# Optimization experiments

Measured on AMD Instinct MI355X. Metric: run time of the kernel, lower is better.

The kernel has to match this reference:

```python
import jax, jax.numpy as jnp
import numpy as np

B, S, HID = 2, 4096, 2048
H, D = 16, 128
BS = 64            # block_size
SR = 0.5           # sparsity_ratio
NB = S // BS       # number of diagonal blocks
SCALE = D ** -0.5


def setup_inputs() -> dict:
    key = jax.random.key(0)
    ks = jax.random.split(key, 7)
    s = 0.02
    return {
        "hidden_states": jax.random.normal(ks[0], (B, S, HID), jnp.float32),
        "Wq": jax.random.normal(ks[1], (HID, H * D), jnp.float32) * s,
        "Wk": jax.random.normal(ks[2], (HID, H * D), jnp.float32) * s,
        "Wv": jax.random.normal(ks[3], (HID, H * D), jnp.float32) * s,
        "Wo": jax.random.normal(ks[4], (H * D, HID), jnp.float32) * s,
        "Wr": jax.random.normal(ks[5], (HID, H), jnp.float32) * s,   # block_router weight
        "br": jax.random.normal(ks[6], (H,), jnp.float32) * s,       # block_router bias
    }


def reference(hidden_states, Wq, Wk, Wv, Wo, Wr, br):
    # projections: torch Linear(x) == x @ W^T; weights stored pre-transposed here
    q = (hidden_states @ Wq).reshape(B, S, H, D).transpose(0, 2, 1, 3)  # [B,H,S,D]
    k = (hidden_states @ Wk).reshape(B, S, H, D).transpose(0, 2, 1, 3)
    v = (hidden_states @ Wv).reshape(B, S, H, D).transpose(0, 2, 1, 3)

    # per-head routing score, mean-pooled over batch (as in torch: routing_scores[:, h].mean())
    routing = jax.nn.sigmoid(hidden_states.mean(axis=1) @ Wr + br)      # [B,H]
    head_score = routing.mean(axis=0)                                   # [H]
    eff_sparsity = SR * (1.0 - head_score * 0.5)
    # torch: max(1, int(block_size * eff)); positive -> floor == int truncation
    attend_count = jnp.maximum(1, jnp.floor(BS * eff_sparsity).astype(jnp.int32))  # [H]

    # block-diagonal attention: only within-block scores are ever finite, so we
    # never materialize the full SxS matrix (softmax over -inf elsewhere is a no-op)
    qb = q.reshape(B, H, NB, BS, D)
    kb = k.reshape(B, H, NB, BS, D)
    vb = v.reshape(B, H, NB, BS, D)
    scores = jnp.einsum("bhnqd,bhnkd->bhnqk", qb, kb) * SCALE           # [B,H,NB,BS,BS]

    # rank of each key within its row (descending); keep == variable-k top-k mask.
    order = jnp.argsort(-scores, axis=-1)
    rank = jnp.argsort(order, axis=-1)
    keep = rank < attend_count[None, :, None, None, None]
    # non-top-k in-block entries are scattered as 0.0 (not -inf) in the original
    masked = jnp.where(keep, scores, 0.0)

    probs = jax.nn.softmax(masked.astype(jnp.float32), axis=-1).astype(q.dtype)
    out_b = jnp.einsum("bhnqk,bhnkd->bhnqd", probs, vb)                 # [B,H,NB,BS,D]
    out = out_b.reshape(B, H, S, D).transpose(0, 2, 1, 3).reshape(B, S, H * D)
    return out @ Wo
```

## Files before the change

kernel.cpp:

```cpp
#include <hip/hip_runtime.h>
#include <hip/hip_bf16.h>
#include <cstdint>
#include <cstddef>

#define B_   2
#define S_   4096
#define HIDN 2048
#define H_   16
#define D_   128
#define NB_  64
#define MTOT 8192
#define QKVN 6144
#define SCALE_ 0.08838834764831845f

typedef unsigned short ushort_t;
typedef __attribute__((ext_vector_type(8))) short short8;
typedef __attribute__((ext_vector_type(8))) ushort_t ushort8;
typedef __attribute__((ext_vector_type(4))) float f32x4;

__device__ inline float b2f(ushort_t x){ union{unsigned u; float f;} v; v.u=((unsigned)x)<<16; return v.f; }
__device__ inline ushort_t f2b(float f){ union{unsigned u; float f;} v; v.f=f; unsigned r=(v.u + 0x7FFF + ((v.u>>16)&1))>>16; return (ushort_t)r; }

#define MFMA_BF16(a,b,c) __builtin_amdgcn_mfma_f32_16x16x32_bf16((a),(b),(c),0,0,0)

__device__ inline void async16(const ushort_t* g, ushort_t* l){
  __builtin_amdgcn_global_load_lds(
      (const __attribute__((address_space(1))) void*)g,
      (__attribute__((address_space(3))) void*)l, 16, 0, 0);
}

__global__ void bsa_convpart(const float* __restrict__ hs, ushort_t* __restrict__ hsB,
                             float* __restrict__ part){
  int t = threadIdx.x;
  int c  = blockIdx.x*512 + t*2;
  int sc = blockIdx.y;
  int b  = blockIdx.z;
  const float* p = hs  + ((size_t)b*S_ + (size_t)sc*128)*HIDN + c;
  ushort_t*    q = hsB + ((size_t)b*S_ + (size_t)sc*128)*HIDN + c;
  float s0=0.f, s1=0.f;
  #pragma unroll 8
  for (int i=0;i<128;i++){
    float2 v = *(const float2*)(p + (size_t)i*HIDN);
    s0 += v.x; s1 += v.y;
    unsigned pk = (unsigned)f2b(v.x) | ((unsigned)f2b(v.y)<<16);
    *(unsigned*)(q + (size_t)i*HIDN) = pk;
  }
  part[((b*32+sc)*HIDN)+c]   = s0;
  part[((b*32+sc)*HIDN)+c+1] = s1;
}

__global__ void bsa_router(const float* __restrict__ part, const float* __restrict__ Wr,
                           const float* __restrict__ br, int* __restrict__ counts){
  __shared__ float cm[2*HIDN];
  __shared__ float sig[2*H_];
  int t = threadIdx.x;
  {
    int b  = t>>9;
    int c4 = (t&511)*4;
    float sx=0.f, sy=0.f, sz=0.f, sw=0.f;
    for (int j=0;j<32;j++){
      float4 v = *(const float4*)&part[((b*32+j)*HIDN)+c4];
      sx+=v.x; sy+=v.y; sz+=v.z; sw+=v.w;
    }
    cm[b*HIDN+c4+0]=sx*(1.0f/S_);
    cm[b*HIDN+c4+1]=sy*(1.0f/S_);
    cm[b*HIDN+c4+2]=sz*(1.0f/S_);
    cm[b*HIDN+c4+3]=sw*(1.0f/S_);
  }
  __syncthreads();
  if (t < 256){
    int g = t>>3;
    int sl = t&7;
    int b = g>>4, h = g&15;
    float acc = 0.f;
    for (int c=sl; c<HIDN; c+=8) acc += cm[b*HIDN+c]*Wr[c*H_+h];
    acc += __shfl_xor(acc, 4);
    acc += __shfl_xor(acc, 2);
    acc += __shfl_xor(acc, 1);
    if (sl==0) sig[g] = 1.f/(1.f+expf(-(acc + br[h])));
  }
  __syncthreads();
  if (t < H_){
    float score = 0.5f*(sig[t] + sig[H_+t]);
    float eff = 0.5f*(1.0f - score*0.5f);
    int ac = (int)floorf(64.f*eff);
    if (ac < 1) ac = 1;
    counts[t] = ac;
  }
}

__global__ void bsa_transpose(const float* w0, const float* w1, const float* w2, const float* w3,
                              ushort_t* o0, ushort_t* o1, ushort_t* o2, ushort_t* o3){
  const float* src; ushort_t* dst;
  switch(blockIdx.z){
    case 0: src=w0; dst=o0; break;
    case 1: src=w1; dst=o1; break;
    case 2: src=w2; dst=o2; break;
    default: src=w3; dst=o3; break;
  }
  __shared__ ushort_t tt[64*72];
  int t = threadIdx.x;
  int r0 = blockIdx.y*64, c0 = blockIdx.x*64;
  #pragma unroll
  for (int it=0; it<16; it++){
    int f = it*256 + t;
    int r = f>>6, c = f&63;
    tt[c*72 + (r ^ ((c&7)<<3))] = f2b(src[(size_t)(r0+r)*HIDN + (c0+c)]);
  }
  __syncthreads();
  #pragma unroll
  for (int it=0; it<2; it++){
    int f = it*256 + t;
    int cc = f>>3, rb = (f&7)<<3;
    ushort8 v = *(const ushort8*)&tt[cc*72 + (rb ^ ((cc&7)<<3))];
    *(ushort8*)&dst[(size_t)(c0+cc)*HIDN + r0 + rb] = v;
  }
}


#define SBAR asm volatile("s_barrier" ::: "memory")
#define WVM6 asm volatile("s_waitcnt vmcnt(6)" ::: "memory")
#define WVM4 asm volatile("s_waitcnt vmcnt(4)" ::: "memory")
#define WVM0 asm volatile("s_waitcnt vmcnt(0)" ::: "memory")
#define PHI  __builtin_amdgcn_s_setprio(1)
#define PLO  __builtin_amdgcn_s_setprio(0)

__device__ __forceinline__ short8 lds_frag(const ushort_t* buf, int row, int kb){
  int off = ((row<<7) + kb) ^ ((row&7)<<4);
  return *(const short8*)((const char*)buf + off);
}

__device__ __forceinline__ void rd_a(short8 (&a)[4][2], const ushort_t* buf, int r0, int l16, int quad){
  #pragma unroll
  for (int mi=0; mi<4; mi++)
    #pragma unroll
    for (int ks=0; ks<2; ks++)
      a[mi][ks] = lds_frag(buf, r0 + mi*16 + l16, ks*64 + quad*16);
}
__device__ __forceinline__ void rd_b(short8 (&b)[2][2], const ushort_t* buf, int r0, int l16, int quad){
  #pragma unroll
  for (int ni=0; ni<2; ni++)
    #pragma unroll
    for (int ks=0; ks<2; ks++)
      b[ni][ks] = lds_frag(buf, r0 + ni*16 + l16, ks*64 + quad*16);
}
__device__ __forceinline__ void mm8(f32x4 (&acc)[8][4], const short8 (&a)[4][2],
                                    const short8 (&b)[2][2], int mo, int no){
  #pragma unroll
  for (int mi=0; mi<4; mi++)
    #pragma unroll
    for (int ni=0; ni<2; ni++){
      acc[mo+mi][no+ni] = MFMA_BF16(a[mi][0], b[ni][0], acc[mo+mi][no+ni]);
      acc[mo+mi][no+ni] = MFMA_BF16(a[mi][1], b[ni][1], acc[mo+mi][no+ni]);
    }
}
__device__ __forceinline__ void stage_half(ushort_t* ldsHalf, const ushort_t* g,
                                           int K, int w, int roff, int coff){
  async16(g + (size_t)(w*16 + roff)*K + coff,     ldsHalf + (w*2+0)*512);
  async16(g + (size_t)(w*16 + 8 + roff)*K + coff, ldsHalf + (w*2+1)*512);
}

template<int F32OUT>
__global__ __launch_bounds__(512, 2) void bsa_gemm8(const ushort_t* __restrict__ A,
                                                    const ushort_t* __restrict__ BT,
                                                    void* __restrict__ Cv,
                                                    int M, int N, int K){
  extern __shared__ __align__(16) ushort_t sm[];
  ushort_t* A0  = sm;
  ushort_t* A1  = sm + 16384;
  ushort_t* Bb0 = sm + 32768;
  ushort_t* Bb1 = sm + 49152;

  int t = threadIdx.x;
  int w = t>>6, lane = t&63, quad = lane>>4, l16 = lane&15;
  int wr = w>>2, wc = w&3;

  int nbx = N>>8;
  int nwg = (M>>8)*nbx;
  int bid = blockIdx.x;
  int swz = (bid&7)*(nwg>>3) + (bid>>3);
  int bx = swz % nbx, by = swz / nbx;
  int m0 = by<<8, n0 = bx<<8;

  const ushort_t* Ag = A  + (size_t)m0*K;
  const ushort_t* Bg = BT + (size_t)n0*K;
  int roff = lane>>3;
  int coff = ((lane&7) ^ roff) << 3;

  f32x4 acc[8][4] = {};
  short8 a[4][2], b0[2][2], b1[2][2];

  stage_half(A0,        Ag,                      K, w, roff, coff);
  stage_half(A0+8192,   Ag + (size_t)128*K,      K, w, roff, coff);
  stage_half(Bb0,       Bg,                      K, w, roff, coff);
  stage_half(Bb0+8192,  Bg + (size_t)128*K,      K, w, roff, coff);
  stage_half(Bb1,       Bg + 64,                 K, w, roff, coff);
  stage_half(Bb1+8192,  Bg + (size_t)128*K + 64, K, w, roff, coff);
  WVM4;
  SBAR;
  rd_b(b0, Bb0, wc*64,     l16, quad);
  rd_b(b1, Bb0, wc*64+32,  l16, quad);

  int nit = K>>7;
  #pragma unroll 1
  for (int i=0; i<nit; i++){
    bool nl = (i+1 < nit);
    int kA  = (2*i+1)<<6;
    int kN0 = (2*i+2)<<6;
    int kN1 = (2*i+3)<<6;
    stage_half(A1, Ag + kA, K, w, roff, coff);
    rd_a(a, A0, wr*128, l16, quad);
    PHI; mm8(acc, a, b0, 0,0); PLO;
    SBAR;
    stage_half(A1+8192, Ag + (size_t)128*K + kA, K, w, roff, coff);
    PHI; mm8(acc, a, b1, 0,2); PLO;
    rd_a(a, A0, wr*128+64, l16, quad);
    SBAR;
    if (nl) stage_half(Bb0, Bg + kN0, K, w, roff, coff);
    PHI; mm8(acc, a, b0, 4,0); PLO;
    if (nl) { WVM6; } else { WVM4; }
    SBAR;
    if (nl) stage_half(Bb0+8192, Bg + (size_t)128*K + kN0, K, w, roff, coff);
    PHI; mm8(acc, a, b1, 4,2); PLO;
    if (nl) { WVM4; } else { WVM0; }
    rd_b(b0, Bb1, wc*64, l16, quad);
    SBAR;
    if (nl) stage_half(A0, Ag + kN0, K, w, roff, coff);
    rd_a(a, A1, wr*128, l16, quad);
    rd_b(b1, Bb1, wc*64+32, l16, quad);
    PHI; mm8(acc, a, b0, 0,0); PLO;
    SBAR;
    if (nl) stage_half(A0+8192, Ag + (size_t)128*K + kN0, K, w, roff, coff);
    PHI; mm8(acc, a, b1, 0,2); PLO;
    rd_a(a, A1, wr*128+64, l16, quad);
    SBAR;
    if (nl) stage_half(Bb1, Bg + kN1, K, w, roff, coff);
    PHI; mm8(acc, a, b0, 4,0); PLO;
    if (nl) { WVM6; }
    SBAR;
    if (nl) stage_half(Bb1+8192, Bg + (size_t)128*K + kN1, K, w, roff, coff);
    PHI; mm8(acc, a, b1, 4,2); PLO;
    if (nl){
      WVM4;
      rd_b(b0, Bb0, wc*64,    l16, quad);
      rd_b(b1, Bb0, wc*64+32, l16, quad);
    }
    SBAR;
  }

  #pragma unroll
  for (int mi=0; mi<8; mi++)
    #pragma unroll
    for (int ni=0; ni<4; ni++){
      int m = m0 + wr*128 + mi*16 + quad*4;
      int n = n0 + wc*64 + ni*16 + l16;
      #pragma unroll
      for (int r=0;r<4;r++){
        if (F32OUT) ((float*)Cv)[(size_t)(m+r)*N + n] = acc[mi][ni][r];
        else        ((ushort_t*)Cv)[(size_t)(m+r)*N + n] = f2b(acc[mi][ni][r]);
      }
    }
}

__global__ __launch_bounds__(256) void bsa_attn(const ushort_t* __restrict__ QKV,
                                                const int* __restrict__ counts,
                                                ushort_t* __restrict__ O){
  __shared__ __align__(16) ushort_t regA[64*136];
  __shared__ __align__(16) ushort_t regB[64*136];
  __shared__ __align__(16) ushort_t Ps[64*72];
  float* Sc = (float*)regA;

  int t = threadIdx.x, w = t>>6, lane = t&63, quad = lane>>4, l16 = lane&15;
  int bid = blockIdx.x;
  int b  = bid>>10;
  int h  = (bid>>6)&15;
  int nb = bid&63;
  size_t qbase = ((size_t)b*S_ + (size_t)nb*64)*QKVN + (size_t)h*D_;
  size_t obase = ((size_t)b*S_ + (size_t)nb*64)*HIDN + (size_t)h*D_;

  int4 vre[4];
  #pragma unroll
  for (int it=0; it<4; it++){
    int f = it*256 + t;
    int r = f>>4, c = (f&15)*8;
    vre[it] = *(const int4*)(QKV + qbase + 4096 + (size_t)r*QKVN + c);
  }

  #pragma unroll
  for (int it=0; it<4; it++){
    int f = it*256 + t;
    int r = f>>4, c = (f&15)*8;
    *(int4*)(&regA[r*136+c]) = *(const int4*)(QKV + qbase +        (size_t)r*QKVN + c);
    *(int4*)(&regB[r*136+c]) = *(const int4*)(QKV + qbase + 2048 + (size_t)r*QKVN + c);
  }
  __syncthreads();

  f32x4 sacc[4] = {};
  #pragma unroll
  for (int ks=0; ks<4; ks++){
    short8 afr = *(const short8*)(&regA[(w*16 + l16)*136 + ks*32 + quad*8]);
    #pragma unroll
    for (int nt=0; nt<4; nt++){
      short8 bfr = *(const short8*)(&regB[(nt*16 + l16)*136 + ks*32 + quad*8]);
      sacc[nt] = MFMA_BF16(afr, bfr, sacc[nt]);
    }
  }
  __syncthreads();

  #pragma unroll
  for (int nt=0; nt<4; nt++)
    #pragma unroll
    for (int r=0;r<4;r++)
      Sc[(w*16 + quad*4 + r)*68 + nt*16 + l16] = sacc[nt][r]*SCALE_;
  #pragma unroll
  for (int it=0; it<4; it++){
    int f = it*256 + t;
    int r = f>>4, c = (f&15)*8;
    *(int4*)(&regB[r*136+c]) = vre[it];
  }

  int cnt = counts[h];
  for (int g=0; g<4; g++){
    float s[4], v[4];
    #pragma unroll
    for (int rr=0; rr<4; rr++){
      s[rr] = Sc[(w*16 + g*4 + rr)*68 + lane];
      v[rr] = s[rr];
    }
    #pragma unroll
    for (int k=2; k<=64; k<<=1){
      #pragma unroll
      for (int m=k>>1; m>=1; m>>=1){
        #pragma unroll
        for (int rr=0; rr<4; rr++){
          float o = __shfl_xor(v[rr], m);
          bool keepMin = (((lane & k)==0) == ((lane & m)==0));
          float lo = fminf(v[rr], o), hi = fmaxf(v[rr], o);
          v[rr] = keepMin ? lo : hi;
        }
      }
    }
    #pragma unroll
    for (int rr=0; rr<4; rr++){
      float T = __shfl(v[rr], 64 - cnt);
      unsigned long long gt = __ballot(s[rr] > T);
      unsigned long long eq = __ballot(s[rr] == T);
      int G = __popcll(gt);
      int eqr = __popcll(eq & ((1ull<<lane)-1ull));
      bool keep = (s[rr] > T) || ((s[rr] == T) && (eqr < cnt - G));
      float m = keep ? s[rr] : 0.0f;
      float mx = fmaxf(__shfl(v[rr], 63), 0.0f);
      float e = __expf(m - mx);
      float sum = e;
      #pragma unroll
      for (int off=32; off; off>>=1) sum += __shfl_xor(sum, off);
      Ps[(w*16 + g*4 + rr)*72 + lane] = f2b(e/sum);
    }
  }
  __syncthreads();

  f32x4 oacc[4][2] = {};
  #pragma unroll
  for (int ks=0; ks<2; ks++){
    short8 bv[2];
    #pragma unroll
    for (int jj=0; jj<2; jj++){
      int n = (w*2+jj)*16 + l16;
      short8 x;
      #pragma unroll
      for (int j=0;j<8;j++){
        int k = ks*32 + quad*8 + j;
        x[j] = (short)regB[k*136 + n];
      }
      bv[jj] = x;
    }
    #pragma unroll
    for (int mt=0; mt<4; mt++){
      short8 aP = *(const short8*)(&Ps[(mt*16 + l16)*72 + ks*32 + quad*8]);
      #pragma unroll
      for (int jj=0; jj<2; jj++)
        oacc[mt][jj] = MFMA_BF16(aP, bv[jj], oacc[mt][jj]);
    }
  }
  #pragma unroll
  for (int mt=0; mt<4; mt++)
    #pragma unroll
    for (int jj=0; jj<2; jj++){
      int row = mt*16 + quad*4;
      int col = (w*2+jj)*16 + l16;
      #pragma unroll
      for (int r=0;r<4;r++)
        O[obase + (size_t)(row+r)*HIDN + col] = f2b(oacc[mt][jj][r]);
    }
}

extern "C" void kernel_launch(void* const* d_in, const int* in_sizes, int n_in,
                              void* d_out, int out_size, void* d_ws, size_t ws_size,
                              hipStream_t stream) {
  const float* hs = (const float*)d_in[0];
  const float* Wq = (const float*)d_in[1];
  const float* Wk = (const float*)d_in[2];
  const float* Wv = (const float*)d_in[3];
  const float* Wo = (const float*)d_in[4];
  const float* Wr = (const float*)d_in[5];
  const float* br = (const float*)d_in[6];
  float* out = (float*)d_out;
  char* ws = (char*)d_ws;

  const size_t MB = 1024u*1024u;
  float*    part   = (float*)(ws + 0);
  int*      counts = (int*)(ws + 512u*1024u);
  ushort_t* hsB    = (ushort_t*)(ws + 1*MB);
  ushort_t* WqT    = (ushort_t*)(ws + 33*MB);
  ushort_t* WkT    = (ushort_t*)(ws + 41*MB);
  ushort_t* WvT    = (ushort_t*)(ws + 49*MB);
  ushort_t* WoT    = (ushort_t*)(ws + 57*MB);
  ushort_t* QKV    = (ushort_t*)(ws + 65*MB);
  ushort_t* AO     = hsB;

  static bool attr_done = false;
  if (!attr_done){
    hipFuncSetAttribute((const void*)&bsa_gemm8<0>,
                        hipFuncAttributeMaxDynamicSharedMemorySize, 131072);
    hipFuncSetAttribute((const void*)&bsa_gemm8<1>,
                        hipFuncAttributeMaxDynamicSharedMemorySize, 131072);
    attr_done = true;
  }

  bsa_convpart  <<<dim3(4,32,2),  256, 0, stream>>>(hs, hsB, part);
  bsa_router    <<<1,            1024, 0, stream>>>(part, Wr, br, counts);
  bsa_transpose <<<dim3(32,32,4), 256, 0, stream>>>(Wq,Wk,Wv,Wo, WqT,WkT,WvT,WoT);
  bsa_gemm8<0><<<dim3(768), 512, 131072, stream>>>(hsB, WqT, (void*)QKV, MTOT, QKVN, 2048);
  bsa_attn      <<<2048,          256, 0, stream>>>(QKV, counts, AO);
  bsa_gemm8<1><<<dim3(256), 512, 131072, stream>>>(AO, WoT, (void*)out, MTOT, 2048, 2048);
}
```

Before: 606.5 us.

## Restructure GEMM main loop into four coarser phases with paired staging

```diff
diff --git a/kernel.cpp b/kernel.cpp
--- a/kernel.cpp
+++ b/kernel.cpp
@@ -119,7 +119,6 @@
 
 
 #define SBAR asm volatile("s_barrier" ::: "memory")
-#define WVM6 asm volatile("s_waitcnt vmcnt(6)" ::: "memory")
 #define WVM4 asm volatile("s_waitcnt vmcnt(4)" ::: "memory")
 #define WVM0 asm volatile("s_waitcnt vmcnt(0)" ::: "memory")
 #define PHI  __builtin_amdgcn_s_setprio(1)
@@ -198,8 +197,6 @@
   stage_half(Bb1+8192,  Bg + (size_t)128*K + 64, K, w, roff, coff);
   WVM4;
   SBAR;
-  rd_b(b0, Bb0, wc*64,     l16, quad);
-  rd_b(b1, Bb0, wc*64+32,  l16, quad);
 
   int nit = K>>7;
   #pragma unroll 1
@@ -208,43 +205,38 @@
     int kA  = (2*i+1)<<6;
     int kN0 = (2*i+2)<<6;
     int kN1 = (2*i+3)<<6;
-    stage_half(A1, Ag + kA, K, w, roff, coff);
-    rd_a(a, A0, wr*128, l16, quad);
-    PHI; mm8(acc, a, b0, 0,0); PLO;
+    stage_half(A1,      Ag + kA,                 K, w, roff, coff);
+    stage_half(A1+8192, Ag + (size_t)128*K + kA, K, w, roff, coff);
+    rd_a(a,  A0,  wr*128,   l16, quad);
+    rd_b(b0, Bb0, wc*64,    l16, quad);
+    rd_b(b1, Bb0, wc*64+32, l16, quad);
+    PHI; mm8(acc, a, b0, 0,0); mm8(acc, a, b1, 0,2); PLO;
     SBAR;
-    stage_half(A1+8192, Ag + (size_t)128*K + kA, K, w, roff, coff);
-    PHI; mm8(acc, a, b1, 0,2); PLO;
+    if (nl){
+      stage_half(Bb0,      Bg + kN0,                 K, w, roff, coff);
+      stage_half(Bb0+8192, Bg + (size_t)128*K + kN0, K, w, roff, coff);
+    }
     rd_a(a, A0, wr*128+64, l16, quad);
+    PHI; mm8(acc, a, b1, 4,2); mm8(acc, a, b0, 4,0); PLO;
+    if (nl) { WVM4; } else { WVM0; }
     SBAR;
-    if (nl) stage_half(Bb0, Bg + kN0, K, w, roff, coff);
-    PHI; mm8(acc, a, b0, 4,0); PLO;
-    if (nl) { WVM6; } else { WVM4; }
+    if (nl){
+      stage_half(A0,      Ag + kN0,                 K, w, roff, coff);
+      stage_half(A0+8192, Ag + (size_t)128*K + kN0, K, w, roff, coff);
+    }
+    rd_a(a,  A1,  wr*128,   l16, quad);
+    rd_b(b0, Bb1, wc*64,    l16, quad);
+    rd_b(b1, Bb1, wc*64+32, l16, quad);
+    PHI; mm8(acc, a, b0, 0,0); mm8(acc, a, b1, 0,2); PLO;
+    if (nl) { WVM4; }
     SBAR;
-    if (nl) stage_half(Bb0+8192, Bg + (size_t)128*K + kN0, K, w, roff, coff);
-    PHI; mm8(acc, a, b1, 4,2); PLO;
-    if (nl) { WVM4; } else { WVM0; }
-    rd_b(b0, Bb1, wc*64, l16, quad);
-    SBAR;
-    if (nl) stage_half(A0, Ag + kN0, K, w, roff, coff);
-    rd_a(a, A1, wr*128, l16, quad);
-    rd_b(b1, Bb1, wc*64+32, l16, quad);
-    PHI; mm8(acc, a, b0, 0,0); PLO;
-    SBAR;
-    if (nl) stage_half(A0+8192, Ag + (size_t)128*K + kN0, K, w, roff, coff);
-    PHI; mm8(acc, a, b1, 0,2); PLO;
+    if (nl){
+      stage_half(Bb1,      Bg + kN1,                 K, w, roff, coff);
+      stage_half(Bb1+8192, Bg + (size_t)128*K + kN1, K, w, roff, coff);
+    }
     rd_a(a, A1, wr*128+64, l16, quad);
-    SBAR;
-    if (nl) stage_half(Bb1, Bg + kN1, K, w, roff, coff);
-    PHI; mm8(acc, a, b0, 4,0); PLO;
-    if (nl) { WVM6; }
-    SBAR;
-    if (nl) stage_half(Bb1+8192, Bg + (size_t)128*K + kN1, K, w, roff, coff);
-    PHI; mm8(acc, a, b1, 4,2); PLO;
-    if (nl){
-      WVM4;
-      rd_b(b0, Bb0, wc*64,    l16, quad);
-      rd_b(b1, Bb0, wc*64+32, l16, quad);
-    }
+    PHI; mm8(acc, a, b1, 4,2); mm8(acc, a, b0, 4,0); PLO;
+    if (nl) { WVM4; }
     SBAR;
   }
 
```

New measurement: 596.8 us. About the same (-1.6%).
